# Kernel optimization log

Measured on AMD Instinct MI355X. Metric: run time of the kernel, lower is better.

The kernel has to match this reference:

```python
import jax, jax.numpy as jnp
import numpy as np

B, T, C = 4, 2048, 1024
E, FF, TOPK = 8, 2048, 2


def setup_inputs() -> dict:
    key = jax.random.key(0)
    k1, k2, k3, k4 = jax.random.split(key, 4)
    s_in = 1.0 / np.sqrt(C)
    s_ff = 1.0 / np.sqrt(FF)
    return {
        "x": jax.random.normal(k1, (B, T, C), dtype=jnp.float32),
        "gate_w": jax.random.normal(k2, (E, C), dtype=jnp.float32) * s_in,
        "w1": jax.random.normal(k3, (E, FF, C), dtype=jnp.float32) * s_in,
        "w2": jax.random.normal(k4, (E, C, FF), dtype=jnp.float32) * s_ff,
    }


def reference(x, gate_w, w1, w2):
    Bq, Tq, Cq = x.shape
    x_flat = x.reshape(-1, Cq)                       # [N, C]
    N = x_flat.shape[0]
    scores = x_flat @ gate_w.T                       # [N, E]
    topk_scores, topk_idx = jax.lax.top_k(scores, TOPK)
    topk_probs = jax.nn.softmax(topk_scores, axis=-1)  # [N, K]
    # combine weights per expert: cw[n, e] = sum_k probs[n,k] * (idx[n,k]==e)
    cw = jnp.zeros((N, E), dtype=x_flat.dtype).at[
        jnp.arange(N)[:, None], topk_idx
    ].add(topk_probs)                                # [N, E]
    y = jnp.zeros_like(x_flat)
    for e in range(E):
        h = jax.nn.silu(x_flat @ w1[e].T) @ w2[e].T  # [N, C]
        y = y + cw[:, e:e + 1] * h
    return y.reshape(Bq, Tq, Cq)
```

## Files before the change

kernel.cpp:

```cpp
#include <hip/hip_runtime.h>
#include <hip/hip_bf16.h>
#include <math.h>

#define NTOK 8192
#define CDIM 1024
#define NEXP 8
#define FFD  2048
#define BM   128
#define RMAX (NTOK*2 + NEXP*BM)

typedef __attribute__((ext_vector_type(8))) short short8;
typedef __attribute__((ext_vector_type(4))) float f32x4;

__device__ __forceinline__ unsigned short f2b(float f){
    __hip_bfloat16 b = __float2bfloat16(f);
    return *reinterpret_cast<unsigned short*>(&b);
}
__device__ __forceinline__ float b2f(unsigned short u){
    __hip_bfloat16 b = *reinterpret_cast<__hip_bfloat16*>(&u);
    return __bfloat162float(b);
}

__device__ __forceinline__ void gl_lds16(const void* g, void* l){
    __builtin_amdgcn_global_load_lds(
        (const __attribute__((address_space(1))) unsigned int*)g,
        (__attribute__((address_space(3))) unsigned int*)l, 16, 0, 0);
}

__global__ void k_cvt(const float* __restrict__ src, unsigned short* __restrict__ dst, int n8){
    int i = blockIdx.x*blockDim.x + threadIdx.x;
    if(i >= n8) return;
    const float4* s = reinterpret_cast<const float4*>(src) + (size_t)i*2;
    float4 a = s[0], b = s[1];
    ushort4 o0 = { f2b(a.x), f2b(a.y), f2b(a.z), f2b(a.w) };
    ushort4 o1 = { f2b(b.x), f2b(b.y), f2b(b.z), f2b(b.w) };
    ushort4* d = reinterpret_cast<ushort4*>(dst) + (size_t)i*2;
    d[0] = o0; d[1] = o1;
}

__global__ void k_gate(const float* __restrict__ x, const float* __restrict__ gw,
                       unsigned short* __restrict__ Xb,
                       int* __restrict__ eidx, float* __restrict__ probs){
    int tok  = blockIdx.x*4 + (threadIdx.x>>6);
    int l    = threadIdx.x & 63;
    const float4* xr  = reinterpret_cast<const float4*>(x + (size_t)tok*CDIM);
    ushort4*      xbw = reinterpret_cast<ushort4*>(Xb + (size_t)tok*CDIM);
    float acc[NEXP];
    #pragma unroll
    for(int e=0;e<NEXP;e++) acc[e]=0.f;
    #pragma unroll
    for(int i=0;i<4;i++){
        float4 v = xr[l + 64*i];
        ushort4 o = { f2b(v.x), f2b(v.y), f2b(v.z), f2b(v.w) };
        xbw[l + 64*i] = o;
        #pragma unroll
        for(int e=0;e<NEXP;e++){
            float4 g = reinterpret_cast<const float4*>(gw + e*CDIM)[l + 64*i];
            acc[e] += v.x*g.x + v.y*g.y + v.z*g.z + v.w*g.w;
        }
    }
    #pragma unroll
    for(int e=0;e<NEXP;e++){
        #pragma unroll
        for(int off=32; off; off>>=1) acc[e] += __shfl_xor(acc[e], off);
    }
    if(l==0){
        int e0=0; float s0=acc[0];
        #pragma unroll
        for(int e=1;e<NEXP;e++) if(acc[e]>s0){s0=acc[e]; e0=e;}
        int e1=-1; float s1=-1e30f;
        #pragma unroll
        for(int e=0;e<NEXP;e++) if(e!=e0 && acc[e]>s1){s1=acc[e]; e1=e;}
        float p0 = 1.f/(1.f + expf(s1-s0));
        float p1 = 1.f - p0;
        eidx[2*tok]=e0;  eidx[2*tok+1]=e1;
        probs[2*tok]=p0; probs[2*tok+1]=p1;
    }
}

__global__ void k_rank(const int* __restrict__ eidx, int* __restrict__ slot,
                       int* __restrict__ aoff, int pad){
    __shared__ int run[NEXP];
    __shared__ int wavehist[16][NEXP];
    int tid  = threadIdx.x;
    int lane = tid & 63, w = tid >> 6;
    if(tid < NEXP) run[tid] = 0;
    __syncthreads();
    for(int iter=0; iter<(2*NTOK)/1024; iter++){
        int t = iter*1024 + tid;
        int e = eidx[t];
        unsigned long long mymask = 0;
        #pragma unroll
        for(int ee=0; ee<NEXP; ee++){
            unsigned long long m = __ballot(e==ee);
            if(ee==e) mymask = m;
            if(lane==0) wavehist[w][ee] = __popcll(m);
        }
        int lanerank = __popcll(mymask & ((1ULL<<lane)-1ULL));
        __syncthreads();
        if(tid < NEXP){
            int base = run[tid];
            #pragma unroll
            for(int ww=0; ww<16; ww++){
                int c = wavehist[ww][tid];
                wavehist[ww][tid] = base;
                base += c;
            }
            run[tid] = base;
        }
        __syncthreads();
        slot[t] = wavehist[w][e] + lanerank;
    }
    __syncthreads();
    if(tid==0){
        int off=0;
        for(int e=0;e<NEXP;e++){ aoff[e]=off; off += (run[e]+pad-1)&~(pad-1); }
        aoff[NEXP]=off;
    }
}

__global__ void k_build(const int* __restrict__ eidx, const int* __restrict__ slot,
                        const int* __restrict__ aoff,
                        int* __restrict__ tor, int* __restrict__ row_of){
    int t = blockIdx.x*blockDim.x + threadIdx.x;
    int e = eidx[t];
    int row = aoff[e] + slot[t];
    tor[row] = t>>1;
    row_of[t] = row;
}

template<bool GATHER, bool SILU>
__global__ __launch_bounds__(256)
void k_gemm_fast(const unsigned short* __restrict__ Abase,
                 const int* __restrict__ tor,
                 const unsigned short* __restrict__ zeropg,
                 const unsigned short* __restrict__ Bbase,
                 const int* __restrict__ aoff,
                 unsigned short* __restrict__ Out,
                 int Kdim, int ldo, int bn_rows)
{
    int row0  = blockIdx.x * BM;
    int total = aoff[NEXP];
    if(row0 >= total) return;
    int e = 0;
    while(e < NEXP-1 && row0 >= aoff[e+1]) e++;
    int col0 = blockIdx.y * 128;

    __shared__ unsigned short sA[128*64];
    __shared__ unsigned short sB[128*64];

    int tid = threadIdx.x;
    int l = tid & 63, w = tid >> 6;
    int wr = w >> 1, wc = w & 1;
    int lr = l & 15;

    int sub = l >> 3, c16 = l & 7;
    int csw = (c16 ^ sub) * 16;
    const char* abase[4];
    const char* bbase[4];
    #pragma unroll
    for(int i=0;i<4;i++){
        int row = w*32 + i*8 + sub;
        if(GATHER){
            int tok = tor[row0 + row];
            abase[i] = (tok>=0) ? (const char*)(Abase + (size_t)tok*Kdim)
                                : (const char*)zeropg;
        } else {
            abase[i] = (const char*)(Abase + (size_t)(row0+row)*Kdim);
        }
        abase[i] += csw;
        bbase[i] = (const char*)(Bbase + ((size_t)e*bn_rows + col0 + row)*Kdim) + csw;
    }

    int kgrp = l >> 4;
    int lsw  = lr & 7;

    f32x4 acc[4][4];
    #pragma unroll
    for(int m=0;m<4;m++)
        #pragma unroll
        for(int n=0;n<4;n++) acc[m][n] = (f32x4){0.f,0.f,0.f,0.f};

    for(int k0=0; k0<Kdim; k0+=64){
        size_t koff = (size_t)k0*2;
        #pragma unroll
        for(int i=0;i<4;i++){
            gl_lds16(abase[i]+koff, (void*)(sA + (w*4+i)*512));
            gl_lds16(bbase[i]+koff, (void*)(sB + (w*4+i)*512));
        }
        __syncthreads();
        __builtin_amdgcn_s_setprio(1);
        #pragma unroll
        for(int kk=0; kk<2; kk++){
            int swc = ((kk<<2) | kgrp) ^ lsw;
            short8 af[4], bfr[4];
            #pragma unroll
            for(int m=0;m<4;m++)
                af[m] = *reinterpret_cast<const short8*>(sA + (wr*64 + m*16 + lr)*64 + swc*8);
            #pragma unroll
            for(int n=0;n<4;n++)
                bfr[n] = *reinterpret_cast<const short8*>(sB + (wc*64 + n*16 + lr)*64 + swc*8);
            #pragma unroll
            for(int m=0;m<4;m++)
                #pragma unroll
                for(int n=0;n<4;n++)
                    acc[m][n] = __builtin_amdgcn_mfma_f32_16x16x32_bf16(af[m], bfr[n], acc[m][n], 0,0,0);
        }
        __builtin_amdgcn_s_setprio(0);
        __syncthreads();
    }

    int orow_base = row0 + wr*64 + (l>>4)*4;
    int ocol_base = col0 + wc*64 + lr;
    #pragma unroll
    for(int m=0;m<4;m++){
        #pragma unroll
        for(int n=0;n<4;n++){
            f32x4 v = acc[m][n];
            #pragma unroll
            for(int j=0;j<4;j++){
                float val = v[j];
                if(SILU) val = val / (1.f + expf(-val));
                size_t idx = (size_t)(orow_base + m*16 + j)*(size_t)ldo + (size_t)(ocol_base + n*16);
                Out[idx] = f2b(val);
            }
        }
    }
}

__global__ void k_combine(const unsigned short* __restrict__ hout,
                          const int* __restrict__ row_of,
                          const float* __restrict__ probs,
                          float* __restrict__ y){
    int i = blockIdx.x*blockDim.x + threadIdx.x;
    int n  = i >> 7;
    int c8 = (i & 127) * 8;
    int r0 = row_of[2*n], r1 = row_of[2*n+1];
    float p0 = probs[2*n], p1 = probs[2*n+1];
    uint4 h0 = *reinterpret_cast<const uint4*>(hout + (size_t)r0*CDIM + c8);
    uint4 h1 = *reinterpret_cast<const uint4*>(hout + (size_t)r1*CDIM + c8);
    const unsigned short* a = reinterpret_cast<const unsigned short*>(&h0);
    const unsigned short* b = reinterpret_cast<const unsigned short*>(&h1);
    float4 o0, o1;
    o0.x = p0*b2f(a[0]) + p1*b2f(b[0]);
    o0.y = p0*b2f(a[1]) + p1*b2f(b[1]);
    o0.z = p0*b2f(a[2]) + p1*b2f(b[2]);
    o0.w = p0*b2f(a[3]) + p1*b2f(b[3]);
    o1.x = p0*b2f(a[4]) + p1*b2f(b[4]);
    o1.y = p0*b2f(a[5]) + p1*b2f(b[5]);
    o1.z = p0*b2f(a[6]) + p1*b2f(b[6]);
    o1.w = p0*b2f(a[7]) + p1*b2f(b[7]);
    float4* dst = reinterpret_cast<float4*>(y + (size_t)n*CDIM + c8);
    dst[0] = o0; dst[1] = o1;
}

extern "C" void kernel_launch(void* const* d_in, const int* in_sizes, int n_in,
                              void* d_out, int out_size, void* d_ws, size_t ws_size,
                              hipStream_t stream){
    const float* x  = (const float*)d_in[0];
    const float* gw = (const float*)d_in[1];
    const float* w1 = (const float*)d_in[2];
    const float* w2 = (const float*)d_in[3];
    float* y = (float*)d_out;
    char* ws = (char*)d_ws;

    int*   aoff   = (int*)(ws + 64);
    int*   eidx   = (int*)(ws + 256);
    float* probs  = (float*)(ws + 256 + 1*65536);
    int*   slot   = (int*)(ws + 256 + 2*65536);
    int*   row_of = (int*)(ws + 256 + 3*65536);
    int*   tor    = (int*)(ws + 256 + 4*65536);
    unsigned short* zeropg = (unsigned short*)(ws + 512*1024);

    const size_t SZ_XB  = (size_t)NTOK*CDIM*2;
    const size_t SZ_W   = (size_t)NEXP*FFD*CDIM*2;
    const size_t CTRL   = 1<<20;

    unsigned short* Xb   = (unsigned short*)(ws + CTRL);
    unsigned short* W1b  = (unsigned short*)(ws + CTRL + SZ_XB);
    unsigned short* W2b  = (unsigned short*)(ws + CTRL + SZ_XB + SZ_W);
    unsigned short* H    = (unsigned short*)(ws + CTRL + SZ_XB + 2*SZ_W);
    unsigned short* hout = Xb;

    hipMemsetAsync(tor, 0xFF, RMAX*sizeof(int), stream);
    hipMemsetAsync(zeropg, 0, 4096, stream);

    int n8 = NEXP*FFD*CDIM/8;
    k_cvt<<<n8/256, 256, 0, stream>>>(w1, W1b, n8);
    k_cvt<<<n8/256, 256, 0, stream>>>(w2, W2b, n8);
    k_gate<<<NTOK/4, 256, 0, stream>>>(x, gw, Xb, eidx, probs);
    k_rank<<<1, 1024, 0, stream>>>(eidx, slot, aoff, BM);
    k_build<<<NTOK*2/256, 256, 0, stream>>>(eidx, slot, aoff, tor, row_of);

    dim3 g1(RMAX/BM, FFD/128);
    k_gemm_fast<true,  true ><<<g1, 256, 0, stream>>>(Xb, tor, zeropg, W1b, aoff, H,    CDIM, FFD,  FFD);
    dim3 g2(RMAX/BM, CDIM/128);
    k_gemm_fast<false, false><<<g2, 256, 0, stream>>>(H,  tor, zeropg, W2b, aoff, hout, FFD,  CDIM, CDIM);

    k_combine<<<NTOK*CDIM/8/256, 256, 0, stream>>>(hout, row_of, probs, y);
}
```

Before: 270.7 us.

## Double-buffer LDS tiles to prefetch next K-slice during MFMA compute

The GEMM main loop now uses two LDS buffers for A and B. It issues the global-to-LDS load for tile t+2 while tile t+1 is in flight, and waits with partial vmcnt counts so compute on the current tile overlaps memory latency. This removes the exposed load latency of the previous load-sync-compute-sync loop. In exchange it doubles LDS use to 64KB per block, which may reduce occupancy, and it relies on hand-placed waitcnt and barrier ordering.

```diff
diff --git a/kernel.cpp b/kernel.cpp
--- a/kernel.cpp
+++ b/kernel.cpp
@@ -146,8 +146,8 @@
     while(e < NEXP-1 && row0 >= aoff[e+1]) e++;
     int col0 = blockIdx.y * 128;
 
-    __shared__ unsigned short sA[128*64];
-    __shared__ unsigned short sB[128*64];
+    __shared__ unsigned short sA[2][128*64];
+    __shared__ unsigned short sB[2][128*64];
 
     int tid = threadIdx.x;
     int l = tid & 63, w = tid >> 6;
@@ -181,14 +181,24 @@
         #pragma unroll
         for(int n=0;n<4;n++) acc[m][n] = (f32x4){0.f,0.f,0.f,0.f};
 
-    for(int k0=0; k0<Kdim; k0+=64){
-        size_t koff = (size_t)k0*2;
-        #pragma unroll
-        for(int i=0;i<4;i++){
-            gl_lds16(abase[i]+koff, (void*)(sA + (w*4+i)*512));
-            gl_lds16(bbase[i]+koff, (void*)(sB + (w*4+i)*512));
-        }
-        __syncthreads();
+    int nt = Kdim/64;
+
+    #pragma unroll
+    for(int i=0;i<4;i++){
+        gl_lds16(abase[i],     (void*)(&sA[0][0] + (w*4+i)*512));
+        gl_lds16(bbase[i],     (void*)(&sB[0][0] + (w*4+i)*512));
+    }
+    #pragma unroll
+    for(int i=0;i<4;i++){
+        gl_lds16(abase[i]+128, (void*)(&sA[1][0] + (w*4+i)*512));
+        gl_lds16(bbase[i]+128, (void*)(&sB[1][0] + (w*4+i)*512));
+    }
+    asm volatile("s_waitcnt vmcnt(8)");
+    __builtin_amdgcn_sched_barrier(0);
+    __builtin_amdgcn_s_barrier();
+
+    for(int t=0; t<nt; ++t){
+        int cur = t & 1;
         __builtin_amdgcn_s_setprio(1);
         #pragma unroll
         for(int kk=0; kk<2; kk++){
@@ -196,10 +206,10 @@
             short8 af[4], bfr[4];
             #pragma unroll
             for(int m=0;m<4;m++)
-                af[m] = *reinterpret_cast<const short8*>(sA + (wr*64 + m*16 + lr)*64 + swc*8);
+                af[m] = *reinterpret_cast<const short8*>(&sA[cur][0] + (wr*64 + m*16 + lr)*64 + swc*8);
             #pragma unroll
             for(int n=0;n<4;n++)
-                bfr[n] = *reinterpret_cast<const short8*>(sB + (wc*64 + n*16 + lr)*64 + swc*8);
+                bfr[n] = *reinterpret_cast<const short8*>(&sB[cur][0] + (wc*64 + n*16 + lr)*64 + swc*8);
             #pragma unroll
             for(int m=0;m<4;m++)
                 #pragma unroll
@@ -207,7 +217,24 @@
                     acc[m][n] = __builtin_amdgcn_mfma_f32_16x16x32_bf16(af[m], bfr[n], acc[m][n], 0,0,0);
         }
         __builtin_amdgcn_s_setprio(0);
-        __syncthreads();
+
+        if(t+1 < nt){
+            __builtin_amdgcn_s_barrier();
+            if(t+2 < nt){
+                size_t koff = (size_t)(t+2)*128;
+                #pragma unroll
+                for(int i=0;i<4;i++){
+                    gl_lds16(abase[i]+koff, (void*)(&sA[cur][0] + (w*4+i)*512));
+                    gl_lds16(bbase[i]+koff, (void*)(&sB[cur][0] + (w*4+i)*512));
+                }
+                asm volatile("s_waitcnt vmcnt(8)");
+            } else {
+                asm volatile("s_waitcnt vmcnt(0)");
+            }
+            __builtin_amdgcn_sched_barrier(0);
+            __builtin_amdgcn_s_barrier();
+            __builtin_amdgcn_sched_barrier(0);
+        }
     }
 
     int orow_base = row0 + wr*64 + (l>>4)*4;
```

New measurement: 308.7 us. +14.0%, slower.
